# Kernel tuning notes

Measured on AMD Instinct MI355X. Metric: run time of the kernel, lower is better.

The kernel has to match this reference:

```python
import jax, jax.numpy as jnp
import numpy as np

N_NODES = 10000
N_EDGES = 320000
F_IN = 128
HID = 32


def sage_mean(x, src, dst, W_self, W_neigh, b, n_nodes):
    # mean aggregation over in-neighbors (messages flow src -> dst)
    msg = x[src]                                   # [E, F]
    agg = jax.ops.segment_sum(msg, dst, num_segments=n_nodes)   # [N, F]
    deg = jax.ops.segment_sum(jnp.ones((src.shape[0],), x.dtype), dst,
                              num_segments=n_nodes)             # [N]
    h_neigh = agg / jnp.maximum(deg, 1.0)[:, None]
    return x @ W_self + h_neigh @ W_neigh + b


def setup_inputs() -> dict:
    key = jax.random.key(0)
    ks = jax.random.split(key, 12)
    s = 0.05
    return {
        "n_feats": jax.random.normal(ks[0], (N_NODES, F_IN), jnp.float32),
        "src": jax.random.randint(ks[1], (N_EDGES,), 0, N_NODES, jnp.int32),
        "dst": jax.random.randint(ks[2], (N_EDGES,), 0, N_NODES, jnp.int32),
        "eps": jax.random.normal(ks[3], (N_NODES, HID), jnp.float32),
        "W1_self": jax.random.normal(ks[4], (F_IN, HID), jnp.float32) * s,
        "W1_neigh": jax.random.normal(ks[5], (F_IN, HID), jnp.float32) * s,
        "b1": jnp.zeros((HID,), jnp.float32),
        "Wmu_self": jax.random.normal(ks[6], (HID, HID), jnp.float32) * s,
        "Wmu_neigh": jax.random.normal(ks[7], (HID, HID), jnp.float32) * s,
        "bmu": jnp.zeros((HID,), jnp.float32),
        "Wls_self": jax.random.normal(ks[8], (HID, HID), jnp.float32) * s,
        "Wls_neigh": jax.random.normal(ks[9], (HID, HID), jnp.float32) * s,
        "bls": jnp.zeros((HID,), jnp.float32),
    }


def reference(n_feats, src, dst, eps, W1_self, W1_neigh, b1,
              Wmu_self, Wmu_neigh, bmu, Wls_self, Wls_neigh, bls):
    n = n_feats.shape[0]
    h = jax.nn.relu(sage_mean(n_feats, src, dst, W1_self, W1_neigh, b1, n))
    mu = sage_mean(h, src, dst, Wmu_self, Wmu_neigh, bmu, n)
    logstd = sage_mean(h, src, dst, Wls_self, Wls_neigh, bls, n)
    z = mu + eps * jnp.exp(logstd)          # reparameterize
    adj = jax.nn.sigmoid(z @ z.T)           # dot-product decode, [N, N]
    return adj, mu, logstd
```

## Files before the change

kernel.cpp:

```cpp
#include <hip/hip_runtime.h>
#include <hip/hip_bf16.h>


#define N_NODES 10000
#define N_EDGES 320000
#define F_IN 128
#define HID 32

__global__ __launch_bounds__(256) void k_gemm_in(
    const float* __restrict__ x, const float* __restrict__ Ws,
    const float* __restrict__ Wn, const float* __restrict__ b,
    float* __restrict__ outS, float* __restrict__ outN) {
  __shared__ float sWs[F_IN * HID];
  __shared__ float sWn[F_IN * HID];
  __shared__ float sx[8 * F_IN];
  const int t = threadIdx.x;
  for (int i = t * 4; i < F_IN * HID; i += 1024) {
    *(float4*)&sWs[i] = *(const float4*)&Ws[i];
    *(float4*)&sWn[i] = *(const float4*)&Wn[i];
  }
  const int row0 = blockIdx.x * 8;
  {
    const int i = t * 4;
    const int r = i >> 7, k = i & 127;
    const int gr = row0 + r;
    float4 v = make_float4(0.f, 0.f, 0.f, 0.f);
    if (gr < N_NODES) v = *(const float4*)&x[gr * F_IN + k];
    *(float4*)&sx[i] = v;
  }
  __syncthreads();
  const int r = t >> 5, c = t & 31;
  const int grow = row0 + r;
  float accS = 0.f, accN = 0.f;
  #pragma unroll 8
  for (int k = 0; k < F_IN; ++k) {
    const float a = sx[r * F_IN + k];
    accS += a * sWs[k * HID + c];
    accN += a * sWn[k * HID + c];
  }
  if (grow < N_NODES) {
    outS[grow * HID + c] = accS + b[c];
    outN[grow * HID + c] = accN;
  }
}

__global__ __launch_bounds__(256) void k_aggregate(
    const float* __restrict__ feat, const int* __restrict__ src,
    const int* __restrict__ dst, float* __restrict__ agg,
    float* __restrict__ deg) {
  const int tid = blockIdx.x * 256 + threadIdx.x;
  const int e = tid >> 5;
  const int k = tid & 31;
  if (e >= N_EDGES) return;
  const int s = src[e];
  const int d = dst[e];
  atomicAdd(&agg[d * HID + k], feat[s * HID + k]);
  if (deg != nullptr && k == 0) atomicAdd(&deg[d], 1.0f);
}

__global__ __launch_bounds__(256) void k_layer1_finish(
    const float* __restrict__ xws, const float* __restrict__ agg,
    const float* __restrict__ deg, float* __restrict__ h) {
  const int i = blockIdx.x * 256 + threadIdx.x;
  if (i >= N_NODES * HID) return;
  const int node = i >> 5;
  float dv = deg[node];
  dv = dv > 1.f ? dv : 1.f;
  const float v = xws[i] + agg[i] / dv;
  h[i] = v > 0.f ? v : 0.f;
}

__global__ __launch_bounds__(256) void k_layer2(
    const float* __restrict__ h, const float* __restrict__ aggh,
    const float* __restrict__ deg, const float* __restrict__ eps,
    const float* __restrict__ Wms, const float* __restrict__ Wmn,
    const float* __restrict__ bm, const float* __restrict__ Wls,
    const float* __restrict__ Wln, const float* __restrict__ bl,
    float* __restrict__ mu_out, float* __restrict__ ls_out,
    float* __restrict__ z) {
  __shared__ float sMs[HID * HID], sMn[HID * HID];
  __shared__ float sLs[HID * HID], sLn[HID * HID];
  __shared__ float sh[8 * HID], shn[8 * HID];
  const int t = threadIdx.x;
  {
    const int i = t * 4;
    *(float4*)&sMs[i] = *(const float4*)&Wms[i];
    *(float4*)&sMn[i] = *(const float4*)&Wmn[i];
    *(float4*)&sLs[i] = *(const float4*)&Wls[i];
    *(float4*)&sLn[i] = *(const float4*)&Wln[i];
  }
  const int node0 = blockIdx.x * 8;
  const int lr = t >> 5;
  const int gnode_ld = node0 + lr;
  if (gnode_ld < N_NODES) {
    float dv = deg[gnode_ld];
    dv = dv > 1.f ? dv : 1.f;
    sh[t] = h[node0 * HID + t];
    shn[t] = aggh[node0 * HID + t] / dv;
  } else {
    sh[t] = 0.f;
    shn[t] = 0.f;
  }
  __syncthreads();
  const int r = t >> 5, c = t & 31;
  const int node = node0 + r;
  float mu = 0.f, ls = 0.f;
  #pragma unroll 8
  for (int k = 0; k < HID; ++k) {
    const float a = sh[r * HID + k];
    const float an = shn[r * HID + k];
    mu += a * sMs[k * HID + c] + an * sMn[k * HID + c];
    ls += a * sLs[k * HID + c] + an * sLn[k * HID + c];
  }
  if (node < N_NODES) {
    mu += bm[c];
    ls += bl[c];
    const int idx = node * HID + c;
    mu_out[idx] = mu;
    ls_out[idx] = ls;
    z[idx] = mu + eps[idx] * __expf(ls);
  }
}

__global__ __launch_bounds__(256) void k_decode(const float* __restrict__ z,
                                                float* __restrict__ adj) {
  __shared__ float za[128][36];
  __shared__ float zb[128][36];
  const int r0 = blockIdx.y * 128;
  const int c0 = blockIdx.x * 128;
  const int t = threadIdx.x;
  for (int i = t; i < 128 * 8; i += 256) {
    const int row = i >> 3, k0 = (i & 7) << 2;
    const int gr = r0 + row;
    const int gc = c0 + row;
    float4 va = make_float4(0.f, 0.f, 0.f, 0.f);
    float4 vb = make_float4(0.f, 0.f, 0.f, 0.f);
    if (gr < N_NODES) va = *(const float4*)&z[gr * HID + k0];
    if (gc < N_NODES) vb = *(const float4*)&z[gc * HID + k0];
    *(float4*)&za[row][k0] = va;
    *(float4*)&zb[row][k0] = vb;
  }
  __syncthreads();
  const int tx = t & 15, ty = t >> 4;
  float acc[8][8];
  #pragma unroll
  for (int i = 0; i < 8; ++i)
    #pragma unroll
    for (int j = 0; j < 8; ++j) acc[i][j] = 0.f;

  #pragma unroll 4
  for (int k = 0; k < HID; ++k) {
    float a[8], b[8];
    #pragma unroll
    for (int i = 0; i < 8; ++i) a[i] = za[ty + i * 16][k];
    #pragma unroll
    for (int j = 0; j < 8; ++j) b[j] = zb[tx + j * 16][k];
    #pragma unroll
    for (int i = 0; i < 8; ++i)
      #pragma unroll
      for (int j = 0; j < 8; ++j) acc[i][j] += a[i] * b[j];
  }

  #pragma unroll
  for (int i = 0; i < 8; ++i) {
    const int r = r0 + ty + i * 16;
    if (r >= N_NODES) continue;
    float* rowp = adj + (size_t)r * N_NODES;
    #pragma unroll
    for (int j = 0; j < 8; ++j) {
      const int c = c0 + tx + j * 16;
      if (c < N_NODES) {
        const float v = acc[i][j];
        rowp[c] = __builtin_amdgcn_rcpf(1.f + __expf(-v));
      }
    }
  }
}

extern "C" void kernel_launch(void* const* d_in, const int* in_sizes, int n_in,
                              void* d_out, int out_size, void* d_ws,
                              size_t ws_size, hipStream_t stream) {
  const float* x   = (const float*)d_in[0];
  const int* src   = (const int*)d_in[1];
  const int* dst   = (const int*)d_in[2];
  const float* eps = (const float*)d_in[3];
  const float* W1s = (const float*)d_in[4];
  const float* W1n = (const float*)d_in[5];
  const float* b1  = (const float*)d_in[6];
  const float* Wms = (const float*)d_in[7];
  const float* Wmn = (const float*)d_in[8];
  const float* bm  = (const float*)d_in[9];
  const float* Wls = (const float*)d_in[10];
  const float* Wln = (const float*)d_in[11];
  const float* bl  = (const float*)d_in[12];

  float* out = (float*)d_out;
  float* adj = out;
  float* mu_out = out + (size_t)N_NODES * N_NODES;
  float* ls_out = mu_out + (size_t)N_NODES * HID;

  float* ws = (float*)d_ws;
  float* deg  = ws;
  float* agg  = ws + N_NODES;
  float* aggh = agg + N_NODES * HID;
  float* xws  = aggh + N_NODES * HID;
  float* xwn  = xws + N_NODES * HID;
  float* h    = xwn + N_NODES * HID;
  float* z    = h + N_NODES * HID;
  (void)ws_size; (void)in_sizes; (void)n_in; (void)out_size;

  hipMemsetAsync(ws, 0, (size_t)(N_NODES + 2 * N_NODES * HID) * sizeof(float),
                 stream);

  k_gemm_in<<<dim3((N_NODES + 7) / 8), dim3(256), 0, stream>>>(x, W1s, W1n, b1,
                                                               xws, xwn);
  k_aggregate<<<dim3((N_EDGES * HID) / 256), dim3(256), 0, stream>>>(
      xwn, src, dst, agg, deg);
  k_layer1_finish<<<dim3((N_NODES * HID) / 256), dim3(256), 0, stream>>>(
      xws, agg, deg, h);
  k_aggregate<<<dim3((N_EDGES * HID) / 256), dim3(256), 0, stream>>>(
      h, src, dst, aggh, nullptr);
  k_layer2<<<dim3((N_NODES + 7) / 8), dim3(256), 0, stream>>>(
      h, aggh, deg, eps, Wms, Wmn, bm, Wls, Wln, bl, mu_out, ls_out, z);
  dim3 dgrid((N_NODES + 127) / 128, (N_NODES + 127) / 128);
  k_decode<<<dgrid, dim3(256), 0, stream>>>(z, adj);
}
```

Measured before the change: 576.3 us.

## Retile decode to 64x64 with XCD-aware block remap; batch 32 rows in input GEMM

Result: no change. 578.3 us (+0.3%).

```diff
diff --git a/kernel.cpp b/kernel.cpp
--- a/kernel.cpp
+++ b/kernel.cpp
@@ -13,34 +13,45 @@
     float* __restrict__ outS, float* __restrict__ outN) {
   __shared__ float sWs[F_IN * HID];
   __shared__ float sWn[F_IN * HID];
-  __shared__ float sx[8 * F_IN];
+  __shared__ float sx[32 * F_IN];
   const int t = threadIdx.x;
+  const int node0 = blockIdx.x * 32;
+  #pragma unroll
   for (int i = t * 4; i < F_IN * HID; i += 1024) {
     *(float4*)&sWs[i] = *(const float4*)&Ws[i];
     *(float4*)&sWn[i] = *(const float4*)&Wn[i];
   }
-  const int row0 = blockIdx.x * 8;
-  {
-    const int i = t * 4;
+  #pragma unroll
+  for (int i = t * 4; i < 32 * F_IN; i += 1024) {
     const int r = i >> 7, k = i & 127;
-    const int gr = row0 + r;
+    const int gr = node0 + r;
     float4 v = make_float4(0.f, 0.f, 0.f, 0.f);
     if (gr < N_NODES) v = *(const float4*)&x[gr * F_IN + k];
     *(float4*)&sx[i] = v;
   }
   __syncthreads();
-  const int r = t >> 5, c = t & 31;
-  const int grow = row0 + r;
-  float accS = 0.f, accN = 0.f;
-  #pragma unroll 8
+  const int c = t & 31, g = t >> 5;
+  float accS[4] = {0.f, 0.f, 0.f, 0.f};
+  float accN[4] = {0.f, 0.f, 0.f, 0.f};
+  #pragma unroll 4
   for (int k = 0; k < F_IN; ++k) {
-    const float a = sx[r * F_IN + k];
-    accS += a * sWs[k * HID + c];
-    accN += a * sWn[k * HID + c];
-  }
-  if (grow < N_NODES) {
-    outS[grow * HID + c] = accS + b[c];
-    outN[grow * HID + c] = accN;
+    const float ws = sWs[k * HID + c];
+    const float wn = sWn[k * HID + c];
+    #pragma unroll
+    for (int m = 0; m < 4; ++m) {
+      const float a = sx[(g + 8 * m) * F_IN + k];
+      accS[m] += a * ws;
+      accN[m] += a * wn;
+    }
+  }
+  const float bc = b[c];
+  #pragma unroll
+  for (int m = 0; m < 4; ++m) {
+    const int node = node0 + g + 8 * m;
+    if (node < N_NODES) {
+      outS[node * HID + c] = accS[m] + bc;
+      outN[node * HID + c] = accN[m];
+    }
   }
 }
 
@@ -122,52 +133,62 @@
   }
 }
 
-__global__ __launch_bounds__(256) void k_decode(const float* __restrict__ z,
-                                                float* __restrict__ adj) {
-  __shared__ float za[128][36];
-  __shared__ float zb[128][36];
-  const int r0 = blockIdx.y * 128;
-  const int c0 = blockIdx.x * 128;
+#define NT_COL 157
+#define NWG (NT_COL * NT_COL)
+#define NWG_Q (NWG / 8)
+#define NWG_R (NWG % 8)
+__global__ __launch_bounds__(256, 4) void k_decode(const float* __restrict__ z,
+                                                   float* __restrict__ adj) {
+  __shared__ float za[64][36];
+  __shared__ float zb[64][36];
+  const int bid = blockIdx.x;
+  const int xcd = bid & 7, idx = bid >> 3;
+  const int wg = (xcd < NWG_R) ? xcd * (NWG_Q + 1) + idx
+                               : NWG_R * (NWG_Q + 1) + (xcd - NWG_R) * NWG_Q + idx;
+  const int rowt = wg / NT_COL, colt = wg % NT_COL;
+  const int r0 = rowt * 64;
+  const int c0 = colt * 64;
   const int t = threadIdx.x;
-  for (int i = t; i < 128 * 8; i += 256) {
-    const int row = i >> 3, k0 = (i & 7) << 2;
+  #pragma unroll
+  for (int i = t; i < 512; i += 256) {
+    const int row = i >> 3, k4 = (i & 7) << 2;
     const int gr = r0 + row;
     const int gc = c0 + row;
     float4 va = make_float4(0.f, 0.f, 0.f, 0.f);
     float4 vb = make_float4(0.f, 0.f, 0.f, 0.f);
-    if (gr < N_NODES) va = *(const float4*)&z[gr * HID + k0];
-    if (gc < N_NODES) vb = *(const float4*)&z[gc * HID + k0];
-    *(float4*)&za[row][k0] = va;
-    *(float4*)&zb[row][k0] = vb;
+    if (gr < N_NODES) va = *(const float4*)&z[gr * HID + k4];
+    if (gc < N_NODES) vb = *(const float4*)&z[gc * HID + k4];
+    *(float4*)&za[row][k4] = va;
+    *(float4*)&zb[row][k4] = vb;
   }
   __syncthreads();
   const int tx = t & 15, ty = t >> 4;
-  float acc[8][8];
-  #pragma unroll
-  for (int i = 0; i < 8; ++i)
-    #pragma unroll
-    for (int j = 0; j < 8; ++j) acc[i][j] = 0.f;
+  float acc[4][4];
+  #pragma unroll
+  for (int i = 0; i < 4; ++i)
+    #pragma unroll
+    for (int j = 0; j < 4; ++j) acc[i][j] = 0.f;
 
   #pragma unroll 4
   for (int k = 0; k < HID; ++k) {
-    float a[8], b[8];
-    #pragma unroll
-    for (int i = 0; i < 8; ++i) a[i] = za[ty + i * 16][k];
-    #pragma unroll
-    for (int j = 0; j < 8; ++j) b[j] = zb[tx + j * 16][k];
-    #pragma unroll
-    for (int i = 0; i < 8; ++i)
+    float a[4], b[4];
+    #pragma unroll
+    for (int i = 0; i < 4; ++i) a[i] = za[ty + i * 16][k];
+    #pragma unroll
+    for (int j = 0; j < 4; ++j) b[j] = zb[tx + j * 16][k];
+    #pragma unroll
+    for (int i = 0; i < 4; ++i)
       #pragma unroll
-      for (int j = 0; j < 8; ++j) acc[i][j] += a[i] * b[j];
-  }
-
-  #pragma unroll
-  for (int i = 0; i < 8; ++i) {
+      for (int j = 0; j < 4; ++j) acc[i][j] += a[i] * b[j];
+  }
+
+  #pragma unroll
+  for (int i = 0; i < 4; ++i) {
     const int r = r0 + ty + i * 16;
     if (r >= N_NODES) continue;
     float* rowp = adj + (size_t)r * N_NODES;
     #pragma unroll
-    for (int j = 0; j < 8; ++j) {
+    for (int j = 0; j < 4; ++j) {
       const int c = c0 + tx + j * 16;
       if (c < N_NODES) {
         const float v = acc[i][j];
@@ -212,8 +233,8 @@
   hipMemsetAsync(ws, 0, (size_t)(N_NODES + 2 * N_NODES * HID) * sizeof(float),
                  stream);
 
-  k_gemm_in<<<dim3((N_NODES + 7) / 8), dim3(256), 0, stream>>>(x, W1s, W1n, b1,
-                                                               xws, xwn);
+  k_gemm_in<<<dim3((N_NODES + 31) / 32), dim3(256), 0, stream>>>(
+      x, W1s, W1n, b1, xws, xwn);
   k_aggregate<<<dim3((N_EDGES * HID) / 256), dim3(256), 0, stream>>>(
       xwn, src, dst, agg, deg);
   k_layer1_finish<<<dim3((N_NODES * HID) / 256), dim3(256), 0, stream>>>(
@@ -222,6 +243,5 @@
       h, src, dst, aggh, nullptr);
   k_layer2<<<dim3((N_NODES + 7) / 8), dim3(256), 0, stream>>>(
       h, aggh, deg, eps, Wms, Wmn, bm, Wls, Wln, bl, mu_out, ls_out, z);
-  dim3 dgrid((N_NODES + 127) / 128, (N_NODES + 127) / 128);
-  k_decode<<<dgrid, dim3(256), 0, stream>>>(z, adj);
-}
+  k_decode<<<dim3(NWG), dim3(256), 0, stream>>>(z, adj);
+}
```
